# Performance work log

Measured on AMD Instinct MI355X. Metric: run time of the kernel, lower is better.

The kernel has to match this reference:

```python
import jax, jax.numpy as jnp
import numpy as np
from jax import lax

N_HEADS = 8
KERNEL = 3
PAD = 1
D_MODEL = 512

def setup_inputs() -> dict:
    key = jax.random.key(0)
    k1, k2, k3 = jax.random.split(key, 3)
    x = jax.random.normal(k1, (64, 1024, D_MODEL), dtype=jnp.float32)
    weight = jax.random.normal(k2, (N_HEADS, 1, KERNEL), dtype=jnp.float32)
    fc_w = jax.random.normal(k3, (D_MODEL, D_MODEL), dtype=jnp.float32) * (1.0 / np.sqrt(D_MODEL))
    return {"x": x, "weight": weight, "fc_w": fc_w}

def reference(x, weight, fc_w):
    bs, gs, d_model = x.shape
    # weight_softmax=True: normalize kernel taps per head
    w = jax.nn.softmax(weight, axis=-1)  # [H, 1, K]
    # view(-1, n_heads, d_model): channels = heads, spatial axis = d_model
    x2 = x.reshape(-1, N_HEADS, d_model)  # [bs*gs/H, H, d_model]
    out = lax.conv_general_dilated(
        x2, w,
        window_strides=(1,),
        padding=[(PAD, PAD)],
        feature_group_count=N_HEADS,
        dimension_numbers=("NCH", "OIH", "NCH"),
    )  # depthwise conv along d_model
    out = out.reshape(bs, gs, d_model)
    # nn.Linear without bias: y = out @ fc_w.T
    return jnp.einsum("bgd,ed->bge", out, fc_w)
```

## Files before the change

kernel.cpp:

```cpp
#include <hip/hip_runtime.h>

typedef __attribute__((ext_vector_type(8))) __bf16  bf16x8;
typedef __attribute__((ext_vector_type(8))) short   short8;
typedef __attribute__((ext_vector_type(4))) float   f32x4;

#define DM   512
#define BM   128
#define BN   128
#define BK   32
#define NNT  4
#define NKT  16
#define TILEB (BN*BK*2)

__device__ __forceinline__ short f2bf(float f) {
  union { float f; unsigned u; } v; v.f = f;
  unsigned r = v.u + 0x7fffu + ((v.u >> 16) & 1u);
  return (short)(r >> 16);
}

__device__ __forceinline__ int swz(int r, int cbyte) {
  return (r * 64 + cbyte) ^ ((r & 3) << 4);
}

__global__ void build_g_kernel(const float* __restrict__ w,
                               const float* __restrict__ fcw,
                               short* __restrict__ Gt) {
  int idx = blockIdx.x * 256 + threadIdx.x;
  int h  = idx >> 15;
  int t  = idx & 32767;
  int e  = t >> 6;
  int d0 = (t & 63) << 3;
  float w0 = w[h*3+0], w1 = w[h*3+1], w2 = w[h*3+2];
  float mx = fmaxf(w0, fmaxf(w1, w2));
  float e0 = __expf(w0-mx), e1 = __expf(w1-mx), e2 = __expf(w2-mx);
  float inv = 1.0f / (e0 + e1 + e2);
  float w0n = e0*inv, w1n = e1*inv, w2n = e2*inv;
  const float* row = fcw + e * DM;
  float v[10];
  v[0] = (d0 > 0) ? row[d0-1] : 0.0f;
  float4 a = *(const float4*)(row + d0);
  float4 b = *(const float4*)(row + d0 + 4);
  v[1]=a.x; v[2]=a.y; v[3]=a.z; v[4]=a.w;
  v[5]=b.x; v[6]=b.y; v[7]=b.z; v[8]=b.w;
  v[9] = (d0 + 8 < DM) ? row[d0+8] : 0.0f;
  short8 sv;
  #pragma unroll
  for (int j = 0; j < 8; ++j)
    sv[j] = f2bf(w1n*v[j+1] + w0n*v[j+2] + w2n*v[j]);
  int nt = e >> 7, r = e & 127;
  int kt = d0 >> 5, c = d0 & 31;
  char* tile = (char*)Gt + (size_t)((h * NNT + nt) * NKT + kt) * TILEB;
  *(short8*)(tile + swz(r, c * 2)) = sv;
}

__global__ __launch_bounds__(256, 4) void gemm_kernel(const float* __restrict__ x,
                                                      const short* __restrict__ Gt,
                                                      float* __restrict__ out) {
  int bid = blockIdx.x;
  int h   = bid & 7;
  int idx = bid >> 3;
  int nt  = idx & 3;
  int mt  = idx >> 2;
  int tid  = threadIdx.x;
  int lane = tid & 63;
  int wid  = tid >> 6;
  int wr = wid >> 1, wc = wid & 1;

  __shared__ short Alds[2][BM * BK];
  __shared__ short Blds[2][BN * BK];

  const char* Bsrc0 = (const char*)Gt + (size_t)(h * NNT + nt) * NKT * TILEB;
  const float* Abase = x + (size_t)(h + 8 * (size_t)mt * BM) * DM;

  float4 ap[4];

  auto loadA = [&](int kt) {
    #pragma unroll
    for (int p = 0; p < 2; ++p) {
      int r = (tid >> 2) + 64 * p;
      const float* xr = Abase + (size_t)r * 8 * DM + kt * BK + (tid & 3) * 8;
      ap[2*p]   = *(const float4*)xr;
      ap[2*p+1] = *(const float4*)(xr + 4);
    }
  };
  auto stageB = [&](int kt, int buf) {
    const char* src = Bsrc0 + kt * TILEB;
    char* dst = (char*)Blds[buf];
    #pragma unroll
    for (int p = 0; p < 2; ++p)
      __builtin_amdgcn_global_load_lds((const void*)(src + p * 4096 + tid * 16),
                                       (void*)(dst + p * 4096 + wid * 1024), 16, 0, 0);
  };
  auto writeA = [&](int buf) {
    char* dst = (char*)Alds[buf];
    #pragma unroll
    for (int p = 0; p < 2; ++p) {
      int r = (tid >> 2) + 64 * p;
      short8 sv;
      sv[0]=f2bf(ap[2*p].x);   sv[1]=f2bf(ap[2*p].y);
      sv[2]=f2bf(ap[2*p].z);   sv[3]=f2bf(ap[2*p].w);
      sv[4]=f2bf(ap[2*p+1].x); sv[5]=f2bf(ap[2*p+1].y);
      sv[6]=f2bf(ap[2*p+1].z); sv[7]=f2bf(ap[2*p+1].w);
      *(short8*)(dst + swz(r, (tid & 3) * 16)) = sv;
    }
  };

  f32x4 acc[4][4] = {};

  auto computeTile = [&](int cur) {
    const char* Ap = (const char*)Alds[cur];
    const char* Bp = (const char*)Blds[cur];
    bf16x8 af[4], bfr[4];
    #pragma unroll
    for (int m = 0; m < 4; ++m)
      af[m] = *(const bf16x8*)(Ap + swz(wr*64 + m*16 + (lane & 15),
                                        (lane >> 4) * 16));
    #pragma unroll
    for (int n = 0; n < 4; ++n)
      bfr[n] = *(const bf16x8*)(Bp + swz(wc*64 + n*16 + (lane & 15),
                                         (lane >> 4) * 16));
    #pragma unroll
    for (int m = 0; m < 4; ++m)
      #pragma unroll
      for (int n = 0; n < 4; ++n)
        acc[m][n] = __builtin_amdgcn_mfma_f32_16x16x32_bf16(af[m], bfr[n], acc[m][n], 0, 0, 0);
  };

  loadA(0);
  stageB(0, 0);
  writeA(0);
  __syncthreads();

  for (int kt = 0; kt < NKT; ++kt) {
    int cur = kt & 1, nxt = cur ^ 1;
    if (kt + 1 < NKT) {
      loadA(kt + 1);
      stageB(kt + 1, nxt);
    }
    computeTile(cur);
    if (kt + 1 < NKT) writeA(nxt);
    __syncthreads();
  }

  int e0 = nt * BN + wc * 64 + (lane & 15);
  #pragma unroll
  for (int m = 0; m < 4; ++m) {
    int tq = mt * BM + wr * 64 + m * 16 + ((lane >> 4) << 2);
    #pragma unroll
    for (int j = 0; j < 4; ++j) {
      int R = h + 8 * (tq + j);
      float* orow = out + (size_t)R * DM + e0;
      #pragma unroll
      for (int n = 0; n < 4; ++n)
        orow[n * 16] = acc[m][n][j];
    }
  }
}

extern "C" void kernel_launch(void* const* d_in, const int* in_sizes, int n_in,
                              void* d_out, int out_size, void* d_ws, size_t ws_size,
                              hipStream_t stream) {
  const float* x   = (const float*)d_in[0];
  const float* w   = (const float*)d_in[1];
  const float* fcw = (const float*)d_in[2];
  float* out = (float*)d_out;
  short* Gt  = (short*)d_ws;

  hipLaunchKernelGGL(build_g_kernel, dim3((8 * DM * DM / 8) / 256), dim3(256), 0, stream,
                     w, fcw, Gt);
  hipLaunchKernelGGL(gemm_kernel, dim3(8 * 64 * NNT), dim3(256), 0, stream,
                     x, Gt, out);
}
```

Baseline: 78.84 us.

## Widen GEMM block tile to 256 output columns to halve A reloads

Each GEMM block now computes two adjacent 128-wide output tiles, sharing one A (x) tile load and bf16 conversion across both. It stages two B tiles per k-step and keeps twice the accumulators, with launch bounds lowered to 2 blocks per CU. The aim is to cut redundant global reads and conversions of x, at the cost of higher register and LDS use and lower occupancy.

```diff
diff --git a/kernel.cpp b/kernel.cpp
--- a/kernel.cpp
+++ b/kernel.cpp
@@ -53,23 +53,24 @@
   *(short8*)(tile + swz(r, c * 2)) = sv;
 }
 
-__global__ __launch_bounds__(256, 4) void gemm_kernel(const float* __restrict__ x,
+__global__ __launch_bounds__(256, 2) void gemm_kernel(const float* __restrict__ x,
                                                       const short* __restrict__ Gt,
                                                       float* __restrict__ out) {
   int bid = blockIdx.x;
   int h   = bid & 7;
   int idx = bid >> 3;
-  int nt  = idx & 3;
-  int mt  = idx >> 2;
+  int nt2 = idx & 1;
+  int mt  = idx >> 1;
   int tid  = threadIdx.x;
   int lane = tid & 63;
   int wid  = tid >> 6;
   int wr = wid >> 1, wc = wid & 1;
+  int ln = lane & 15, sf = lane >> 4;
 
-  __shared__ short Alds[2][BM * BK];
-  __shared__ short Blds[2][BN * BK];
+  __shared__ char Alds[2][TILEB];
+  __shared__ char Blds[2][2 * TILEB];
 
-  const char* Bsrc0 = (const char*)Gt + (size_t)(h * NNT + nt) * NKT * TILEB;
+  const char* Bsrc0 = (const char*)Gt + (size_t)((h * NNT + nt2 * 2) * NKT) * TILEB;
   const float* Abase = x + (size_t)(h + 8 * (size_t)mt * BM) * DM;
 
   float4 ap[4];
@@ -84,15 +85,19 @@
     }
   };
   auto stageB = [&](int kt, int buf) {
-    const char* src = Bsrc0 + kt * TILEB;
-    char* dst = (char*)Blds[buf];
+    char* dst = Blds[buf];
     #pragma unroll
-    for (int p = 0; p < 2; ++p)
-      __builtin_amdgcn_global_load_lds((const void*)(src + p * 4096 + tid * 16),
-                                       (void*)(dst + p * 4096 + wid * 1024), 16, 0, 0);
+    for (int t = 0; t < 2; ++t) {
+      const char* src = Bsrc0 + ((size_t)t * NKT + kt) * TILEB;
+      #pragma unroll
+      for (int p = 0; p < 2; ++p)
+        __builtin_amdgcn_global_load_lds((const void*)(src + p * 4096 + tid * 16),
+                                         (void*)(dst + t * TILEB + p * 4096 + wid * 1024),
+                                         16, 0, 0);
+    }
   };
   auto writeA = [&](int buf) {
-    char* dst = (char*)Alds[buf];
+    char* dst = Alds[buf];
     #pragma unroll
     for (int p = 0; p < 2; ++p) {
       int r = (tid >> 2) + 64 * p;
@@ -105,24 +110,23 @@
     }
   };
 
-  f32x4 acc[4][4] = {};
+  f32x4 acc[4][8] = {};
 
   auto computeTile = [&](int cur) {
-    const char* Ap = (const char*)Alds[cur];
-    const char* Bp = (const char*)Blds[cur];
-    bf16x8 af[4], bfr[4];
+    const char* Ap = Alds[cur];
+    const char* Bp = Blds[cur];
+    bf16x8 af[4], bfr[8];
     #pragma unroll
     for (int m = 0; m < 4; ++m)
-      af[m] = *(const bf16x8*)(Ap + swz(wr*64 + m*16 + (lane & 15),
-                                        (lane >> 4) * 16));
+      af[m] = *(const bf16x8*)(Ap + swz(wr*64 + m*16 + ln, sf * 16));
     #pragma unroll
-    for (int n = 0; n < 4; ++n)
-      bfr[n] = *(const bf16x8*)(Bp + swz(wc*64 + n*16 + (lane & 15),
-                                         (lane >> 4) * 16));
+    for (int n = 0; n < 8; ++n)
+      bfr[n] = *(const bf16x8*)(Bp + (n >> 2) * TILEB
+                                   + swz(wc*64 + (n & 3)*16 + ln, sf * 16));
     #pragma unroll
     for (int m = 0; m < 4; ++m)
       #pragma unroll
-      for (int n = 0; n < 4; ++n)
+      for (int n = 0; n < 8; ++n)
         acc[m][n] = __builtin_amdgcn_mfma_f32_16x16x32_bf16(af[m], bfr[n], acc[m][n], 0, 0, 0);
   };
 
@@ -142,17 +146,18 @@
     __syncthreads();
   }
 
-  int e0 = nt * BN + wc * 64 + (lane & 15);
   #pragma unroll
   for (int m = 0; m < 4; ++m) {
-    int tq = mt * BM + wr * 64 + m * 16 + ((lane >> 4) << 2);
+    int tq = mt * BM + wr * 64 + m * 16 + (sf << 2);
     #pragma unroll
     for (int j = 0; j < 4; ++j) {
       int R = h + 8 * (tq + j);
-      float* orow = out + (size_t)R * DM + e0;
+      float* orow = out + (size_t)R * DM;
       #pragma unroll
-      for (int n = 0; n < 4; ++n)
-        orow[n * 16] = acc[m][n][j];
+      for (int n = 0; n < 8; ++n) {
+        int e0 = nt2 * 256 + (n >> 2) * 128 + wc * 64 + (n & 3) * 16 + ln;
+        orow[e0] = acc[m][n][j];
+      }
     }
   }
 }
@@ -168,6 +173,6 @@
 
   hipLaunchKernelGGL(build_g_kernel, dim3((8 * DM * DM / 8) / 256), dim3(256), 0, stream,
                      w, fcw, Gt);
-  hipLaunchKernelGGL(gemm_kernel, dim3(8 * 64 * NNT), dim3(256), 0, stream,
+  hipLaunchKernelGGL(gemm_kernel, dim3(8 * 64 * 2), dim3(256), 0, stream,
                      x, Gt, out);
 }
```

Result: slower. 83.03 us (+5.3%).
